# Kernel tuning notes

Measured on AMD Instinct MI355X. Metric: run time of the kernel, lower is better.

The kernel has to match this reference:

```python
import jax, jax.numpy as jnp
import numpy as np

N = 50000   # nodes
E = 800000  # edges
D = 128     # hidden_dim
O = 128     # out_dim (must equal hidden_dim; see prior_mean Linear)
T = 16      # number of timesteps for the modeled time encoding
EPS = 1e-9


def _gcn(x, W, b, src, dst, ew, n):
    """PyG-style GCNConv: add self-loops, symmetric deg^-1/2 normalization."""
    loop = jnp.arange(n)
    s = jnp.concatenate([src, loop])
    d = jnp.concatenate([dst, loop])
    w = jnp.concatenate([ew, jnp.ones((n,), x.dtype)])
    deg = jax.ops.segment_sum(w, d, num_segments=n)
    dinv = jnp.where(deg > 0, jax.lax.rsqrt(deg), 0.0)
    norm = dinv[s] * w * dinv[d]              # [E+N]
    h = x @ W                                  # [N, out]
    out = jax.ops.segment_sum(h[s] * norm[:, None], d, num_segments=n)
    return out + b


def setup_inputs() -> dict:
    key = jax.random.key(0)
    ks = jax.random.split(key, 20)

    def lin(k, fan_in, fan_out):
        return jax.random.normal(k, (fan_in, fan_out), jnp.float32) / np.sqrt(fan_in)

    return {
        "edge_index": jax.random.randint(ks[0], (2, E), 0, N, dtype=jnp.int64),
        "x": jax.random.normal(ks[1], (N, D), jnp.float32),
        "t": 3,
        "edge_score": jax.random.uniform(ks[2], (E,), jnp.float32),
        "total_len": 16,
        "train_len": 12,
        "W_enc": lin(ks[3], D, D), "b_enc": jnp.zeros((D,), jnp.float32),
        "W_mu": lin(ks[4], D, O), "b_mu": jnp.zeros((O,), jnp.float32),
        "W_std": lin(ks[5], D, O), "b_std": jnp.zeros((O,), jnp.float32),
        "W_prior": lin(ks[6], D, O), "b_prior": jnp.zeros((O,), jnp.float32),
        "W_pm": lin(ks[7], D, O), "b_pm": jnp.zeros((O,), jnp.float32),
        "W_ps": lin(ks[8], D, O), "b_ps": jnp.zeros((O,), jnp.float32),
        "time_emb": 0.02 * jax.random.normal(ks[9], (T, O), jnp.float32),
    }


def reference(edge_index, x, t, edge_score, total_len, train_len,
              W_enc, b_enc, W_mu, b_mu, W_std, b_std,
              W_prior, b_prior, W_pm, b_pm, W_ps, b_ps, time_emb):
    src, dst = edge_index[0], edge_index[1]
    n = x.shape[0]
    ones_e = jnp.ones((src.shape[0],), x.dtype)

    # encoder
    enc_t = jax.nn.relu(_gcn(x, W_enc, b_enc, src, dst, edge_score, n))
    # drop = 0.0 -> dropout is identity
    enc_mean_t = _gcn(enc_t, W_mu, b_mu, src, dst, ones_e, n)
    enc_std_t = jax.nn.sigmoid(_gcn(enc_t, W_std, b_std, src, dst, ones_e, n))

    # reparameterize (fixed eps for determinism)
    eps = jax.random.normal(jax.random.key(42), enc_mean_t.shape, enc_mean_t.dtype)
    conf_z_t = eps * enc_std_t + enc_mean_t

    # prior branch: time_encoding(prior, t) modeled as additive time embedding
    prior = jax.nn.relu(_gcn(x, W_prior, b_prior, src, dst, ones_e, n))
    prior = prior + time_emb[t]
    prior_mean = prior @ W_pm + b_pm
    prior_std = jax.nn.sigmoid(prior @ W_ps + b_ps)

    # fused KL divergence
    kl = (2.0 * jnp.log(prior_std + EPS) - 2.0 * jnp.log(enc_std_t + EPS)
          + ((enc_std_t + EPS) ** 2 + (enc_mean_t - prior_mean) ** 2)
          / (prior_std + EPS) ** 2 - 1.0)
    kl_loss = 0.5 * jnp.mean(jnp.sum(kl, axis=1), axis=0)
    return kl_loss, conf_z_t
```

## Files before the change

### kernel.cpp

```cpp
#include <hip/hip_runtime.h>
#include <math.h>

#define D 128

typedef unsigned int u32;
typedef unsigned short u16;
typedef __attribute__((ext_vector_type(8))) short bf16x8;
typedef __attribute__((ext_vector_type(4))) float f32x4;
typedef __attribute__((ext_vector_type(4))) u32 u32x4;

__device__ __forceinline__ u32 rotl32(u32 x, int r){ return (x<<r) | (x>>(32-r)); }

__device__ __forceinline__ u16 f2bf(float x){
  u32 u = __float_as_uint(x);
  return (u16)((u + 0x7fffu + ((u >> 16) & 1u)) >> 16);
}
__device__ __forceinline__ float bf2f(u16 h){ return __uint_as_float(((u32)h) << 16); }

__device__ __forceinline__ float jax_normal_part_xor(u32 m){
  const u32 ks0 = 0u, ks1 = 42u, ks2 = 0x1BD11BF0u;
  u32 x0 = 0u + ks0;
  u32 x1 = m  + ks1;
  #define TF_R4(a,b,c,d) \
    x0 += x1; x1 = rotl32(x1,(a)); x1 ^= x0; \
    x0 += x1; x1 = rotl32(x1,(b)); x1 ^= x0; \
    x0 += x1; x1 = rotl32(x1,(c)); x1 ^= x0; \
    x0 += x1; x1 = rotl32(x1,(d)); x1 ^= x0;
  TF_R4(13,15,26,6)   x0 += ks1; x1 += ks2 + 1u;
  TF_R4(17,29,16,24)  x0 += ks2; x1 += ks0 + 2u;
  TF_R4(13,15,26,6)   x0 += ks0; x1 += ks1 + 3u;
  TF_R4(17,29,16,24)  x0 += ks1; x1 += ks2 + 4u;
  TF_R4(13,15,26,6)   x0 += ks2; x1 += ks0 + 5u;
  #undef TF_R4
  u32 bits = x0 ^ x1;
  float f = __uint_as_float((bits >> 9) | 0x3F800000u) - 1.0f;
  const float LO = -0.99999994f;
  float u = fmaxf(LO, f * 2.0f + LO);
  float w = -__logf(fmaf(-u, u, 1.0f));
  float p;
  if (w < 5.0f){
    w -= 2.5f;
    p =  2.81022636e-08f;
    p = fmaf(p, w,  3.43273939e-07f);
    p = fmaf(p, w, -3.5233877e-06f);
    p = fmaf(p, w, -4.39150654e-06f);
    p = fmaf(p, w,  0.00021858087f);
    p = fmaf(p, w, -0.00125372503f);
    p = fmaf(p, w, -0.00417768164f);
    p = fmaf(p, w,  0.246640727f);
    p = fmaf(p, w,  1.50140941f);
  } else {
    w = sqrtf(w) - 3.0f;
    p = -0.000200214257f;
    p = fmaf(p, w,  0.000100950558f);
    p = fmaf(p, w,  0.00134934322f);
    p = fmaf(p, w, -0.00367342844f);
    p = fmaf(p, w,  0.00573950773f);
    p = fmaf(p, w, -0.0076224613f);
    p = fmaf(p, w,  0.00943887047f);
    p = fmaf(p, w,  1.00167406f);
    p = fmaf(p, w,  2.83297682f);
  }
  return 1.41421354f * (p * u);
}

__device__ __forceinline__ float sigmoidf_(float z){ return 1.0f / (1.0f + __expf(-z)); }

__global__ void k_detect(const u32* __restrict__ e_u32, int* __restrict__ flag){
  __shared__ int s_nz;
  if (threadIdx.x == 0) s_nz = 0;
  __syncthreads();
  if (e_u32[2*threadIdx.x + 1] != 0u) atomicAdd(&s_nz, 1);
  __syncthreads();
  if (threadIdx.x == 0) *flag = (s_nz == 0) ? 1 : 0;
}

__global__ void k_norm(const void* __restrict__ eidx, const int* __restrict__ flag,
                       int* __restrict__ src_w, int* __restrict__ dst_w, int e){
  int i = blockIdx.x*256 + threadIdx.x;
  if (i >= e) return;
  if (*flag){
    const u32* u = (const u32*)eidx;
    src_w[i] = (int)u[2*(size_t)i];
    dst_w[i] = (int)u[2*((size_t)e + i)];
  } else {
    const int* p = (const int*)eidx;
    src_w[i] = p[i];
    dst_w[i] = p[e + i];
  }
}

__global__ void k_init(int* __restrict__ cnt, int n){
  int i = blockIdx.x*256 + threadIdx.x;
  if (i < n) cnt[i] = 0;
}

__global__ void k_hist(const int* __restrict__ dst, int* __restrict__ cnt, int e){
  int i = blockIdx.x*256 + threadIdx.x;
  if (i >= e) return;
  atomicAdd(&cnt[dst[i]], 1);
}

__global__ __launch_bounds__(256) void k_scan1(const int* __restrict__ cnt,
                                               int* __restrict__ rp,
                                               int* __restrict__ bsum, int n){
  __shared__ int sh[256];
  int tid = threadIdx.x, idx = blockIdx.x*256 + tid;
  int v = (idx < n) ? cnt[idx] : 0;
  sh[tid] = v; __syncthreads();
  for (int off = 1; off < 256; off <<= 1){
    int t = (tid >= off) ? sh[tid-off] : 0;
    __syncthreads(); sh[tid] += t; __syncthreads();
  }
  if (idx < n) rp[idx] = sh[tid] - v;
  if (tid == 255) bsum[blockIdx.x] = sh[255];
}

__global__ __launch_bounds__(1024) void k_scan2(int* __restrict__ bsum, int nb){
  __shared__ int sh[1024];
  int tid = threadIdx.x;
  int v = (tid < nb) ? bsum[tid] : 0;
  sh[tid] = v; __syncthreads();
  for (int off = 1; off < 1024; off <<= 1){
    int t = (tid >= off) ? sh[tid-off] : 0;
    __syncthreads(); sh[tid] += t; __syncthreads();
  }
  if (tid < nb) bsum[tid] = sh[tid] - v;
}

__global__ void k_scan3(int* __restrict__ rp, int* __restrict__ cur,
                        const int* __restrict__ bsum, const int* __restrict__ cnt,
                        float* __restrict__ dinv_o, int n, int e){
  int idx = blockIdx.x*256 + threadIdx.x;
  if (idx < n){
    int r = rp[idx] + bsum[blockIdx.x];
    rp[idx] = r; cur[idx] = r;
    dinv_o[idx] = rsqrtf((float)(cnt[idx] + 1));
  }
  if (idx == 0) rp[n] = e;
}

__global__ void k_scatter(const int* __restrict__ src, const int* __restrict__ dst,
                          const float* __restrict__ sc, int* __restrict__ cur,
                          int* __restrict__ col, float* __restrict__ wsrt, int e){
  int i = blockIdx.x*256 + threadIdx.x;
  if (i >= e) return;
  int d = dst[i];
  int p = atomicAdd(&cur[d], 1);
  col[p] = src[i];
  wsrt[p] = sc[i];
}

__global__ void k_deg(const int* __restrict__ rp, const float* __restrict__ wsrt,
                      float* __restrict__ dinv_s, int n){
  int i = blockIdx.x*256 + threadIdx.x;
  if (i >= n) return;
  float s = 1.0f;
  int e0 = rp[i], e1 = rp[i+1];
  for (int j = e0; j < e1; ++j) s += wsrt[j];
  dinv_s[i] = rsqrtf(s);
}

__global__ void k_wconv(const float* __restrict__ W0, const float* __restrict__ W1,
                        const float* __restrict__ W2, const float* __restrict__ W3,
                        const float* __restrict__ W4, const float* __restrict__ W5,
                        u16* __restrict__ wt){
  const float* Ws[6] = {W0,W1,W2,W3,W4,W5};
  const float* W = Ws[blockIdx.y];
  u16* Wt = wt + (size_t)blockIdx.y*16384;
  int idx = blockIdx.x*256 + threadIdx.x;
  int k = idx >> 7, col = idx & 127;
  Wt[col*128 + k] = f2bf(W[idx]);
}

__global__ __launch_bounds__(256) void k_agg_dual(
    const float* __restrict__ x, const int* __restrict__ rp,
    const int* __restrict__ col, const float* __restrict__ wsrt,
    const float* __restrict__ dinv_s, const float* __restrict__ dinv_o,
    u16* __restrict__ out_s, u16* __restrict__ out_o, int n){
  int wid = (blockIdx.x * 256 + threadIdx.x) >> 6;
  int lane = threadIdx.x & 63;
  if (wid >= n) return;
  const float2* x2 = (const float2*)x;
  float dsv = dinv_s[wid], dov = dinv_o[wid];
  float2 xv = x2[(size_t)wid*64 + lane];
  float ss = dsv*dsv, oo = dov*dov;
  float2 as = { xv.x*ss, xv.y*ss };
  float2 ao = { xv.x*oo, xv.y*oo };
  int e0 = rp[wid], e1 = rp[wid+1];
  for (int base = e0; base < e1; base += 64){
    int cnt = e1 - base; if (cnt > 64) cnt = 64;
    int idx = base + (lane < cnt ? lane : cnt - 1);
    int   sl = col[idx];
    float wl = wsrt[idx];
    float nsl = dinv_s[sl] * wl * dsv;
    float nol = dinv_o[sl] * dov;
    int j = 0;
    for (; j + 4 <= cnt; j += 4){
      int   s0=__shfl(sl,j),   s1=__shfl(sl,j+1),   s2=__shfl(sl,j+2),   s3=__shfl(sl,j+3);
      float a0=__shfl(nsl,j),  a1=__shfl(nsl,j+1),  a2=__shfl(nsl,j+2),  a3=__shfl(nsl,j+3);
      float b0=__shfl(nol,j),  b1=__shfl(nol,j+1),  b2=__shfl(nol,j+2),  b3=__shfl(nol,j+3);
      float2 r0 = x2[(size_t)s0*64 + lane];
      float2 r1 = x2[(size_t)s1*64 + lane];
      float2 r2 = x2[(size_t)s2*64 + lane];
      float2 r3 = x2[(size_t)s3*64 + lane];
      as.x = fmaf(a0,r0.x,as.x); as.y = fmaf(a0,r0.y,as.y);
      ao.x = fmaf(b0,r0.x,ao.x); ao.y = fmaf(b0,r0.y,ao.y);
      as.x = fmaf(a1,r1.x,as.x); as.y = fmaf(a1,r1.y,as.y);
      ao.x = fmaf(b1,r1.x,ao.x); ao.y = fmaf(b1,r1.y,ao.y);
      as.x = fmaf(a2,r2.x,as.x); as.y = fmaf(a2,r2.y,as.y);
      ao.x = fmaf(b2,r2.x,ao.x); ao.y = fmaf(b2,r2.y,ao.y);
      as.x = fmaf(a3,r3.x,as.x); as.y = fmaf(a3,r3.y,as.y);
      ao.x = fmaf(b3,r3.x,ao.x); ao.y = fmaf(b3,r3.y,ao.y);
    }
    for (; j < cnt; ++j){
      int   s0=__shfl(sl,j);
      float a0=__shfl(nsl,j), b0=__shfl(nol,j);
      float2 r0 = x2[(size_t)s0*64 + lane];
      as.x = fmaf(a0,r0.x,as.x); as.y = fmaf(a0,r0.y,as.y);
      ao.x = fmaf(b0,r0.x,ao.x); ao.y = fmaf(b0,r0.y,ao.y);
    }
  }
  ((u32*)out_s)[(size_t)wid*64 + lane] = (u32)f2bf(as.x) | ((u32)f2bf(as.y) << 16);
  ((u32*)out_o)[(size_t)wid*64 + lane] = (u32)f2bf(ao.x) | ((u32)f2bf(ao.y) << 16);
}

__global__ __launch_bounds__(256) void k_agg_one(
    const u16* __restrict__ h, const int* __restrict__ rp,
    const int* __restrict__ col, const float* __restrict__ dinv_o,
    u16* __restrict__ out, int n){
  int wid = (blockIdx.x * 256 + threadIdx.x) >> 6;
  int lane = threadIdx.x & 63;
  if (wid >= n) return;
  const u32* h2 = (const u32*)h;
  float dov = dinv_o[wid];
  u32 hv = h2[(size_t)wid*64 + lane];
  float oo = dov*dov;
  float2 ao = { bf2f((u16)(hv & 0xffff))*oo, bf2f((u16)(hv >> 16))*oo };
  int e0 = rp[wid], e1 = rp[wid+1];
  for (int base = e0; base < e1; base += 64){
    int cnt = e1 - base; if (cnt > 64) cnt = 64;
    int idx = base + (lane < cnt ? lane : cnt - 1);
    int   sl = col[idx];
    float nol = dinv_o[sl] * dov;
    int j = 0;
    for (; j + 4 <= cnt; j += 4){
      int   s0=__shfl(sl,j),  s1=__shfl(sl,j+1),  s2=__shfl(sl,j+2),  s3=__shfl(sl,j+3);
      float b0=__shfl(nol,j), b1=__shfl(nol,j+1), b2=__shfl(nol,j+2), b3=__shfl(nol,j+3);
      u32 r0 = h2[(size_t)s0*64 + lane];
      u32 r1 = h2[(size_t)s1*64 + lane];
      u32 r2 = h2[(size_t)s2*64 + lane];
      u32 r3 = h2[(size_t)s3*64 + lane];
      ao.x = fmaf(b0, bf2f((u16)(r0&0xffff)), ao.x); ao.y = fmaf(b0, bf2f((u16)(r0>>16)), ao.y);
      ao.x = fmaf(b1, bf2f((u16)(r1&0xffff)), ao.x); ao.y = fmaf(b1, bf2f((u16)(r1>>16)), ao.y);
      ao.x = fmaf(b2, bf2f((u16)(r2&0xffff)), ao.x); ao.y = fmaf(b2, bf2f((u16)(r2>>16)), ao.y);
      ao.x = fmaf(b3, bf2f((u16)(r3&0xffff)), ao.x); ao.y = fmaf(b3, bf2f((u16)(r3>>16)), ao.y);
    }
    for (; j < cnt; ++j){
      int   s0=__shfl(sl,j);
      float b0=__shfl(nol,j);
      u32 r0 = h2[(size_t)s0*64 + lane];
      ao.x = fmaf(b0, bf2f((u16)(r0&0xffff)), ao.x); ao.y = fmaf(b0, bf2f((u16)(r0>>16)), ao.y);
    }
  }
  ((u32*)out)[(size_t)wid*64 + lane] = (u32)f2bf(ao.x) | ((u32)f2bf(ao.y) << 16);
}


__global__ __launch_bounds__(256) void k_mfma_act2(
    const u16* __restrict__ A0, const u16* __restrict__ Wt0, const float* __restrict__ b0,
    const u16* __restrict__ A1, const u16* __restrict__ Wt1, const float* __restrict__ b1,
    const float* __restrict__ temb, const int* __restrict__ t_ptr,
    u16* __restrict__ out0, u16* __restrict__ out1, int n){
  const int sl = blockIdx.y;
  const u16* A  = sl ? A1 : A0;
  const u16* Wt = sl ? Wt1 : Wt0;
  const float* b = sl ? b1 : b0;
  u16* out = sl ? out1 : out0;
  const int tid = threadIdx.x;
  const int lane = tid & 63, wave = tid >> 6;
  const int lr = lane & 15, lg = lane >> 4;
  const int row0 = blockIdx.x * 64;
  int rowf = row0 + wave*16 + lr;
  int rowc = rowf < n ? rowf : n - 1;
  const char* Arow = (const char*)A + (size_t)rowc*256;
  const char* Wb   = (const char*)Wt + lg*16;
  f32x4 z = {0.f,0.f,0.f,0.f};
  f32x4 acc[8];
  #pragma unroll
  for (int i = 0; i < 8; ++i) acc[i] = z;
  #pragma unroll
  for (int ks = 0; ks < 4; ++ks){
    bf16x8 a = *(const bf16x8*)(Arow + ks*64 + lg*16);
    #pragma unroll
    for (int cf = 0; cf < 8; ++cf){
      bf16x8 bb = *(const bf16x8*)(Wb + (cf*16 + lr)*256 + ks*64);
      acc[cf] = __builtin_amdgcn_mfma_f32_16x16x32_bf16(a, bb, acc[cf], 0, 0, 0);
    }
  }
  int t = sl ? *t_ptr : 0;
  int rbase = row0 + wave*16 + (lg << 2);
  #pragma unroll
  for (int cf = 0; cf < 8; ++cf){
    int colw = cf*16 + lr;
    float bb = b[colw];
    float tt = sl ? temb[t*128 + colw] : 0.f;
    #pragma unroll
    for (int r = 0; r < 4; ++r){
      int row = rbase + r;
      if (row < n)
        out[(size_t)row*128 + colw] = f2bf(fmaxf(acc[cf][r] + bb, 0.f) + tt);
    }
  }
}

__global__ __launch_bounds__(256) void k_mfma_dual(
    const u16* __restrict__ A, const u16* __restrict__ Wt1, const float* __restrict__ b1,
    const u16* __restrict__ Wt2, const float* __restrict__ b2,
    u32* __restrict__ pmps, int n){
  const int tid = threadIdx.x;
  const int lane = tid & 63, wave = tid >> 6;
  const int lr = lane & 15, lg = lane >> 4;
  const int row0 = blockIdx.x * 64;
  int rowf = row0 + wave*16 + lr;
  int rowc = rowf < n ? rowf : n - 1;
  const char* Arow = (const char*)A + (size_t)rowc*256;
  const char* W1b  = (const char*)Wt1 + lg*16;
  const char* W2b  = (const char*)Wt2 + lg*16;
  f32x4 z = {0.f,0.f,0.f,0.f};
  f32x4 acc1[8], acc2[8];
  #pragma unroll
  for (int i = 0; i < 8; ++i){ acc1[i] = z; acc2[i] = z; }
  #pragma unroll
  for (int ks = 0; ks < 4; ++ks){
    bf16x8 a = *(const bf16x8*)(Arow + ks*64 + lg*16);
    #pragma unroll
    for (int cf = 0; cf < 8; ++cf){
      int off = (cf*16 + lr)*256 + ks*64;
      bf16x8 bb1 = *(const bf16x8*)(W1b + off);
      acc1[cf] = __builtin_amdgcn_mfma_f32_16x16x32_bf16(a, bb1, acc1[cf], 0, 0, 0);
      bf16x8 bb2 = *(const bf16x8*)(W2b + off);
      acc2[cf] = __builtin_amdgcn_mfma_f32_16x16x32_bf16(a, bb2, acc2[cf], 0, 0, 0);
    }
  }
  int rbase = row0 + wave*16 + (lg << 2);
  #pragma unroll
  for (int cf = 0; cf < 8; ++cf){
    int colw = cf*16 + lr;
    float bb1 = b1[colw], bb2 = b2[colw];
    #pragma unroll
    for (int r = 0; r < 4; ++r){
      int row = rbase + r;
      if (row < n){
        u16 pmh = f2bf(acc1[cf][r] + bb1);
        u16 psh = f2bf(sigmoidf_(acc2[cf][r] + bb2));
        pmps[(size_t)row*128 + colw] = (u32)pmh | ((u32)psh << 16);
      }
    }
  }
}

__global__ __launch_bounds__(256) void k_mfma_final(
    const u16* __restrict__ A, const u16* __restrict__ Wtmu, const float* __restrict__ bmu,
    const u16* __restrict__ Wtstd, const float* __restrict__ bstd,
    const u32* __restrict__ pmps,
    float* __restrict__ conf, float* __restrict__ pblk, int n){
  const int tid = threadIdx.x;
  const int lane = tid & 63, wave = tid >> 6;
  const int lr = lane & 15, lg = lane >> 4;
  const int row0 = blockIdx.x * 64;
  int rowf = row0 + wave*16 + lr;
  int rowc = rowf < n ? rowf : n - 1;
  const char* Arow = (const char*)A + (size_t)rowc*256;
  const char* W1b  = (const char*)Wtmu + lg*16;
  const char* W2b  = (const char*)Wtstd + lg*16;
  f32x4 z = {0.f,0.f,0.f,0.f};
  f32x4 acc1[8], acc2[8];
  #pragma unroll
  for (int i = 0; i < 8; ++i){ acc1[i] = z; acc2[i] = z; }
  #pragma unroll
  for (int ks = 0; ks < 4; ++ks){
    bf16x8 a = *(const bf16x8*)(Arow + ks*64 + lg*16);
    #pragma unroll
    for (int cf = 0; cf < 8; ++cf){
      int off = (cf*16 + lr)*256 + ks*64;
      bf16x8 bb1 = *(const bf16x8*)(W1b + off);
      acc1[cf] = __builtin_amdgcn_mfma_f32_16x16x32_bf16(a, bb1, acc1[cf], 0, 0, 0);
      bf16x8 bb2 = *(const bf16x8*)(W2b + off);
      acc2[cf] = __builtin_amdgcn_mfma_f32_16x16x32_bf16(a, bb2, acc2[cf], 0, 0, 0);
    }
  }
  const float EPS = 1e-9f;
  int rbase = row0 + wave*16 + (lg << 2);
  float klsum = 0.f;
  #pragma unroll
  for (int cf = 0; cf < 8; ++cf){
    int colw = cf*16 + lr;
    float bb1 = bmu[colw], bb2 = bstd[colw];
    #pragma unroll
    for (int r = 0; r < 4; ++r){
      int row = rbase + r;
      if (row < n){
        size_t m = (size_t)row*128 + colw;
        float em = acc1[cf][r] + bb1;
        float es = sigmoidf_(acc2[cf][r] + bb2);
        float eps = jax_normal_part_xor((u32)m);
        conf[m] = fmaf(eps, es, em);
        u32 pp = pmps[m];
        float pmv = bf2f((u16)(pp & 0xffff)), psv = bf2f((u16)(pp >> 16));
        float es_e = es + EPS, ps_e = psv + EPS;
        float diff = em - pmv;
        klsum += 2.0f*__logf(ps_e/es_e)
               + (es_e*es_e + diff*diff) / (ps_e*ps_e) - 1.0f;
      }
    }
  }
  #pragma unroll
  for (int off = 32; off > 0; off >>= 1) klsum += __shfl_down(klsum, off);
  __shared__ float wsum[4];
  if ((tid & 63) == 0) wsum[tid >> 6] = klsum;
  __syncthreads();
  if (tid == 0) pblk[blockIdx.x] = wsum[0] + wsum[1] + wsum[2] + wsum[3];
}

__global__ __launch_bounds__(256) void k_finish(const float* __restrict__ pblk, int nb,
                                                float* __restrict__ out0, int n){
  __shared__ double sh[256];
  double s = 0.0;
  for (int i = threadIdx.x; i < nb; i += 256) s += (double)pblk[i];
  sh[threadIdx.x] = s; __syncthreads();
  for (int off = 128; off > 0; off >>= 1){
    if (threadIdx.x < off) sh[threadIdx.x] += sh[threadIdx.x + off];
    __syncthreads();
  }
  if (threadIdx.x == 0) out0[0] = (float)(0.5 * sh[0] / (double)n);
}

extern "C" void kernel_launch(void* const* d_in, const int* in_sizes, int n_in,
                              void* d_out, int out_size, void* d_ws, size_t ws_size,
                              hipStream_t stream){
  const void*  eidx   = d_in[0];
  const float* x      = (const float*)d_in[1];
  const int*   t_ptr  = (const int*)d_in[2];
  const float* escore = (const float*)d_in[3];
  const float* W_enc = (const float*)d_in[6];  const float* b_enc = (const float*)d_in[7];
  const float* W_mu  = (const float*)d_in[8];  const float* b_mu  = (const float*)d_in[9];
  const float* W_std = (const float*)d_in[10]; const float* b_std = (const float*)d_in[11];
  const float* W_pr  = (const float*)d_in[12]; const float* b_pr  = (const float*)d_in[13];
  const float* W_pm  = (const float*)d_in[14]; const float* b_pm  = (const float*)d_in[15];
  const float* W_ps  = (const float*)d_in[16]; const float* b_ps  = (const float*)d_in[17];
  const float* temb  = (const float*)d_in[18];

  const int N = in_sizes[1] / D;
  const int E = in_sizes[3];

  char* w = (char*)d_ws;
  auto alloc = [&](size_t bytes) -> char* {
    char* p = w; w += (bytes + 255) & ~(size_t)255; return p;
  };
  int*    flag   = (int*)   alloc(256);
  int*    src_w  = (int*)   alloc((size_t)E*4);
  int*    dst_w  = (int*)   alloc((size_t)E*4);
  int*    cnt    = (int*)   alloc((size_t)N*4);
  int*    rp     = (int*)   alloc((size_t)(N+1)*4);
  int*    cur    = (int*)   alloc((size_t)N*4);
  float*  dinv_s = (float*) alloc((size_t)N*4);
  float*  dinv_o = (float*) alloc((size_t)N*4);
  int*    bsum   = (int*)   alloc(1024*4);
  int*    col    = (int*)   alloc((size_t)E*4);
  float*  wsrt   = (float*) alloc((size_t)E*4);
  u16*    wt     = (u16*)   alloc((size_t)6*16384*2);
  u16*    B1     = (u16*)   alloc((size_t)N*D*2);
  u16*    B2     = (u16*)   alloc((size_t)N*D*2);
  u16*    B3     = (u16*)   alloc((size_t)N*D*2);
  u32*    PMPS   = (u32*)   alloc((size_t)N*D*4);
  u16*    B5     = (u16*)   alloc((size_t)N*D*2);
  const int gG64 = (N + 63) / 64;
  float*  pblk   = (float*) alloc((size_t)gG64*4);
  (void)ws_size; (void)n_in; (void)out_size;

  float* conf = ((float*)d_out) + 1;

  u16* Wt_enc = wt + 0*16384;
  u16* Wt_pr  = wt + 1*16384;
  u16* Wt_pm  = wt + 2*16384;
  u16* Wt_ps  = wt + 3*16384;
  u16* Wt_mu  = wt + 4*16384;
  u16* Wt_std = wt + 5*16384;

  const int gE  = (E + 255) / 256;
  const int gN  = (N + 255) / 256;
  const int gW  = (N * 64 + 255) / 256;

  k_wconv <<<dim3(64,6), 256, 0, stream>>>(W_enc, W_pr, W_pm, W_ps, W_mu, W_std, wt);
  k_detect <<<1, 256, 0, stream>>>((const u32*)eidx, flag);
  k_norm   <<<gE, 256, 0, stream>>>(eidx, flag, src_w, dst_w, E);
  k_init   <<<gN, 256, 0, stream>>>(cnt, N);
  k_hist   <<<gE, 256, 0, stream>>>(dst_w, cnt, E);
  k_scan1  <<<gN, 256, 0, stream>>>(cnt, rp, bsum, N);
  k_scan2  <<<1, 1024, 0, stream>>>(bsum, gN);
  k_scan3  <<<gN, 256, 0, stream>>>(rp, cur, bsum, cnt, dinv_o, N, E);
  k_scatter<<<gE, 256, 0, stream>>>(src_w, dst_w, escore, cur, col, wsrt, E);
  k_deg    <<<gN, 256, 0, stream>>>(rp, wsrt, dinv_s, N);

  k_agg_dual<<<gW, 256, 0, stream>>>(x, rp, col, wsrt, dinv_s, dinv_o, B1, B2, N);
  k_mfma_act2<<<dim3(gG64,2), 256, 0, stream>>>(B1, Wt_enc, b_enc, B2, Wt_pr, b_pr,
                                                temb, t_ptr, B3, B5, N);
  k_agg_one<<<gW, 256, 0, stream>>>(B3, rp, col, dinv_o, B2, N);
  k_mfma_dual<<<gG64, 256, 0, stream>>>(B5, Wt_pm, b_pm, Wt_ps, b_ps, PMPS, N);
  k_mfma_final<<<gG64, 256, 0, stream>>>(B2, Wt_mu, b_mu, Wt_std, b_std, PMPS,
                                         conf, pblk, N);
  k_finish<<<1, 256, 0, stream>>>(pblk, gG64, (float*)d_out, N);
}
```

Before: 384.3 us.

## Fuse prior head GEMMs into KL kernel and precompute bf16 noise

Merges the prior mean/std GEMM kernel into the final KL kernel so the packed prior buffer is no longer written and re-read. Moves the Threefry normal-noise generation into a separate kernel that stores eps as packed bf16, and retiles the MFMA kernels to 32 rows per block with waves split across column halves. This adds an extra eps buffer write and read and rounds the noise to bf16, reducing accuracy of conf_z.

```diff
diff --git a/kernel.cpp b/kernel.cpp
--- a/kernel.cpp
+++ b/kernel.cpp
@@ -66,6 +66,17 @@
 
 __device__ __forceinline__ float sigmoidf_(float z){ return 1.0f / (1.0f + __expf(-z)); }
 
+__global__ __launch_bounds__(256) void k_eps(u32* __restrict__ epsb, int half_total){
+  int idx = blockIdx.x*256 + threadIdx.x;
+  int stride = gridDim.x*256;
+  for (int i = idx; i < half_total; i += stride){
+    u32 m0 = 2u*(u32)i;
+    float e0 = jax_normal_part_xor(m0);
+    float e1 = jax_normal_part_xor(m0 + 1u);
+    epsb[i] = (u32)f2bf(e0) | ((u32)f2bf(e1) << 16);
+  }
+}
+
 __global__ void k_detect(const u32* __restrict__ e_u32, int* __restrict__ flag){
   __shared__ int s_nz;
   if (threadIdx.x == 0) s_nz = 0;
@@ -280,29 +291,30 @@
   const int tid = threadIdx.x;
   const int lane = tid & 63, wave = tid >> 6;
   const int lr = lane & 15, lg = lane >> 4;
-  const int row0 = blockIdx.x * 64;
-  int rowf = row0 + wave*16 + lr;
+  const int rw = wave >> 1, cw = wave & 1;
+  const int row0 = blockIdx.x*32 + rw*16;
+  int rowf = row0 + lr;
   int rowc = rowf < n ? rowf : n - 1;
   const char* Arow = (const char*)A + (size_t)rowc*256;
-  const char* Wb   = (const char*)Wt + lg*16;
+  const char* Wb   = (const char*)Wt + (cw*64 + lr)*256 + lg*16;
   f32x4 z = {0.f,0.f,0.f,0.f};
-  f32x4 acc[8];
-  #pragma unroll
-  for (int i = 0; i < 8; ++i) acc[i] = z;
+  f32x4 acc[4];
+  #pragma unroll
+  for (int i = 0; i < 4; ++i) acc[i] = z;
   #pragma unroll
   for (int ks = 0; ks < 4; ++ks){
     bf16x8 a = *(const bf16x8*)(Arow + ks*64 + lg*16);
     #pragma unroll
-    for (int cf = 0; cf < 8; ++cf){
-      bf16x8 bb = *(const bf16x8*)(Wb + (cf*16 + lr)*256 + ks*64);
+    for (int cf = 0; cf < 4; ++cf){
+      bf16x8 bb = *(const bf16x8*)(Wb + cf*16*256 + ks*64);
       acc[cf] = __builtin_amdgcn_mfma_f32_16x16x32_bf16(a, bb, acc[cf], 0, 0, 0);
     }
   }
   int t = sl ? *t_ptr : 0;
-  int rbase = row0 + wave*16 + (lg << 2);
-  #pragma unroll
-  for (int cf = 0; cf < 8; ++cf){
-    int colw = cf*16 + lr;
+  int rbase = row0 + (lg << 2);
+  #pragma unroll
+  for (int cf = 0; cf < 4; ++cf){
+    int colw = cw*64 + cf*16 + lr;
     float bb = b[colw];
     float tt = sl ? temb[t*128 + colw] : 0.f;
     #pragma unroll
@@ -314,100 +326,65 @@
   }
 }
 
-__global__ __launch_bounds__(256) void k_mfma_dual(
-    const u16* __restrict__ A, const u16* __restrict__ Wt1, const float* __restrict__ b1,
-    const u16* __restrict__ Wt2, const float* __restrict__ b2,
-    u32* __restrict__ pmps, int n){
-  const int tid = threadIdx.x;
-  const int lane = tid & 63, wave = tid >> 6;
-  const int lr = lane & 15, lg = lane >> 4;
-  const int row0 = blockIdx.x * 64;
-  int rowf = row0 + wave*16 + lr;
-  int rowc = rowf < n ? rowf : n - 1;
-  const char* Arow = (const char*)A + (size_t)rowc*256;
-  const char* W1b  = (const char*)Wt1 + lg*16;
-  const char* W2b  = (const char*)Wt2 + lg*16;
-  f32x4 z = {0.f,0.f,0.f,0.f};
-  f32x4 acc1[8], acc2[8];
-  #pragma unroll
-  for (int i = 0; i < 8; ++i){ acc1[i] = z; acc2[i] = z; }
-  #pragma unroll
-  for (int ks = 0; ks < 4; ++ks){
-    bf16x8 a = *(const bf16x8*)(Arow + ks*64 + lg*16);
-    #pragma unroll
-    for (int cf = 0; cf < 8; ++cf){
-      int off = (cf*16 + lr)*256 + ks*64;
-      bf16x8 bb1 = *(const bf16x8*)(W1b + off);
-      acc1[cf] = __builtin_amdgcn_mfma_f32_16x16x32_bf16(a, bb1, acc1[cf], 0, 0, 0);
-      bf16x8 bb2 = *(const bf16x8*)(W2b + off);
-      acc2[cf] = __builtin_amdgcn_mfma_f32_16x16x32_bf16(a, bb2, acc2[cf], 0, 0, 0);
-    }
-  }
-  int rbase = row0 + wave*16 + (lg << 2);
-  #pragma unroll
-  for (int cf = 0; cf < 8; ++cf){
-    int colw = cf*16 + lr;
-    float bb1 = b1[colw], bb2 = b2[colw];
-    #pragma unroll
-    for (int r = 0; r < 4; ++r){
-      int row = rbase + r;
-      if (row < n){
-        u16 pmh = f2bf(acc1[cf][r] + bb1);
-        u16 psh = f2bf(sigmoidf_(acc2[cf][r] + bb2));
-        pmps[(size_t)row*128 + colw] = (u32)pmh | ((u32)psh << 16);
-      }
-    }
-  }
-}
-
-__global__ __launch_bounds__(256) void k_mfma_final(
-    const u16* __restrict__ A, const u16* __restrict__ Wtmu, const float* __restrict__ bmu,
-    const u16* __restrict__ Wtstd, const float* __restrict__ bstd,
-    const u32* __restrict__ pmps,
+__global__ __launch_bounds__(256) void k_mfma_quad(
+    const u16* __restrict__ Apr, const u16* __restrict__ Aen,
+    const u16* __restrict__ Wtpm, const float* __restrict__ bpm,
+    const u16* __restrict__ Wtps, const float* __restrict__ bps,
+    const u16* __restrict__ Wtmu, const float* __restrict__ bmu,
+    const u16* __restrict__ Wtsd, const float* __restrict__ bsd,
+    const u32* __restrict__ epsb,
     float* __restrict__ conf, float* __restrict__ pblk, int n){
   const int tid = threadIdx.x;
   const int lane = tid & 63, wave = tid >> 6;
   const int lr = lane & 15, lg = lane >> 4;
-  const int row0 = blockIdx.x * 64;
-  int rowf = row0 + wave*16 + lr;
+  const int rw = wave >> 1, cw = wave & 1;
+  const int row0 = blockIdx.x*32 + rw*16;
+  int rowf = row0 + lr;
   int rowc = rowf < n ? rowf : n - 1;
-  const char* Arow = (const char*)A + (size_t)rowc*256;
-  const char* W1b  = (const char*)Wtmu + lg*16;
-  const char* W2b  = (const char*)Wtstd + lg*16;
+  const char* Ap = (const char*)Apr + (size_t)rowc*256;
+  const char* Ae = (const char*)Aen + (size_t)rowc*256;
+  const int wcb = (cw*64 + lr)*256 + lg*16;
+  const char* Wpm = (const char*)Wtpm + wcb;
+  const char* Wps = (const char*)Wtps + wcb;
+  const char* Wmu = (const char*)Wtmu + wcb;
+  const char* Wsd = (const char*)Wtsd + wcb;
   f32x4 z = {0.f,0.f,0.f,0.f};
-  f32x4 acc1[8], acc2[8];
-  #pragma unroll
-  for (int i = 0; i < 8; ++i){ acc1[i] = z; acc2[i] = z; }
+  f32x4 aPM[4], aPS[4], aMU[4], aSD[4];
+  #pragma unroll
+  for (int i = 0; i < 4; ++i){ aPM[i]=z; aPS[i]=z; aMU[i]=z; aSD[i]=z; }
   #pragma unroll
   for (int ks = 0; ks < 4; ++ks){
-    bf16x8 a = *(const bf16x8*)(Arow + ks*64 + lg*16);
+    bf16x8 a5 = *(const bf16x8*)(Ap + ks*64 + lg*16);
+    bf16x8 a2 = *(const bf16x8*)(Ae + ks*64 + lg*16);
     #pragma unroll
-    for (int cf = 0; cf < 8; ++cf){
-      int off = (cf*16 + lr)*256 + ks*64;
-      bf16x8 bb1 = *(const bf16x8*)(W1b + off);
-      acc1[cf] = __builtin_amdgcn_mfma_f32_16x16x32_bf16(a, bb1, acc1[cf], 0, 0, 0);
-      bf16x8 bb2 = *(const bf16x8*)(W2b + off);
-      acc2[cf] = __builtin_amdgcn_mfma_f32_16x16x32_bf16(a, bb2, acc2[cf], 0, 0, 0);
+    for (int cf = 0; cf < 4; ++cf){
+      int off = cf*16*256 + ks*64;
+      aPM[cf] = __builtin_amdgcn_mfma_f32_16x16x32_bf16(a5, *(const bf16x8*)(Wpm+off), aPM[cf], 0,0,0);
+      aPS[cf] = __builtin_amdgcn_mfma_f32_16x16x32_bf16(a5, *(const bf16x8*)(Wps+off), aPS[cf], 0,0,0);
+      aMU[cf] = __builtin_amdgcn_mfma_f32_16x16x32_bf16(a2, *(const bf16x8*)(Wmu+off), aMU[cf], 0,0,0);
+      aSD[cf] = __builtin_amdgcn_mfma_f32_16x16x32_bf16(a2, *(const bf16x8*)(Wsd+off), aSD[cf], 0,0,0);
     }
   }
   const float EPS = 1e-9f;
-  int rbase = row0 + wave*16 + (lg << 2);
+  int rbase = row0 + (lg << 2);
   float klsum = 0.f;
   #pragma unroll
-  for (int cf = 0; cf < 8; ++cf){
-    int colw = cf*16 + lr;
-    float bb1 = bmu[colw], bb2 = bstd[colw];
+  for (int cf = 0; cf < 4; ++cf){
+    int colw = cw*64 + cf*16 + lr;
+    float bb1 = bpm[colw], bb2 = bps[colw];
+    float bb3 = bmu[colw], bb4 = bsd[colw];
     #pragma unroll
     for (int r = 0; r < 4; ++r){
       int row = rbase + r;
       if (row < n){
         size_t m = (size_t)row*128 + colw;
-        float em = acc1[cf][r] + bb1;
-        float es = sigmoidf_(acc2[cf][r] + bb2);
-        float eps = jax_normal_part_xor((u32)m);
+        float pmv = aPM[cf][r] + bb1;
+        float psv = sigmoidf_(aPS[cf][r] + bb2);
+        float em  = aMU[cf][r] + bb3;
+        float es  = sigmoidf_(aSD[cf][r] + bb4);
+        u32 ew = epsb[m >> 1];
+        float eps = bf2f((u16)((colw & 1) ? (ew >> 16) : (ew & 0xffff)));
         conf[m] = fmaf(eps, es, em);
-        u32 pp = pmps[m];
-        float pmv = bf2f((u16)(pp & 0xffff)), psv = bf2f((u16)(pp >> 16));
         float es_e = es + EPS, ps_e = psv + EPS;
         float diff = em - pmv;
         klsum += 2.0f*__logf(ps_e/es_e)
@@ -473,10 +450,10 @@
   u16*    B1     = (u16*)   alloc((size_t)N*D*2);
   u16*    B2     = (u16*)   alloc((size_t)N*D*2);
   u16*    B3     = (u16*)   alloc((size_t)N*D*2);
-  u32*    PMPS   = (u32*)   alloc((size_t)N*D*4);
   u16*    B5     = (u16*)   alloc((size_t)N*D*2);
-  const int gG64 = (N + 63) / 64;
-  float*  pblk   = (float*) alloc((size_t)gG64*4);
+  u32*    EPSB   = (u32*)   alloc((size_t)N*64*4);
+  const int gG32 = (N + 31) / 32;
+  float*  pblk   = (float*) alloc((size_t)gG32*4);
   (void)ws_size; (void)n_in; (void)out_size;
 
   float* conf = ((float*)d_out) + 1;
@@ -492,7 +469,8 @@
   const int gN  = (N + 255) / 256;
   const int gW  = (N * 64 + 255) / 256;
 
-  k_wconv <<<dim3(64,6), 256, 0, stream>>>(W_enc, W_pr, W_pm, W_ps, W_mu, W_std, wt);
+  k_eps    <<<2048, 256, 0, stream>>>(EPSB, N*64);
+  k_wconv  <<<dim3(64,6), 256, 0, stream>>>(W_enc, W_pr, W_pm, W_ps, W_mu, W_std, wt);
   k_detect <<<1, 256, 0, stream>>>((const u32*)eidx, flag);
   k_norm   <<<gE, 256, 0, stream>>>(eidx, flag, src_w, dst_w, E);
   k_init   <<<gN, 256, 0, stream>>>(cnt, N);
@@ -504,11 +482,11 @@
   k_deg    <<<gN, 256, 0, stream>>>(rp, wsrt, dinv_s, N);
 
   k_agg_dual<<<gW, 256, 0, stream>>>(x, rp, col, wsrt, dinv_s, dinv_o, B1, B2, N);
-  k_mfma_act2<<<dim3(gG64,2), 256, 0, stream>>>(B1, Wt_enc, b_enc, B2, Wt_pr, b_pr,
+  k_mfma_act2<<<dim3(gG32,2), 256, 0, stream>>>(B1, Wt_enc, b_enc, B2, Wt_pr, b_pr,
                                                 temb, t_ptr, B3, B5, N);
   k_agg_one<<<gW, 256, 0, stream>>>(B3, rp, col, dinv_o, B2, N);
-  k_mfma_dual<<<gG64, 256, 0, stream>>>(B5, Wt_pm, b_pm, Wt_ps, b_ps, PMPS, N);
-  k_mfma_final<<<gG64, 256, 0, stream>>>(B2, Wt_mu, b_mu, Wt_std, b_std, PMPS,
-                                         conf, pblk, N);
-  k_finish<<<1, 256, 0, stream>>>(pblk, gG64, (float*)d_out, N);
-}
+  k_mfma_quad<<<gG32, 256, 0, stream>>>(B5, B2, Wt_pm, b_pm, Wt_ps, b_ps,
+                                        Wt_mu, b_mu, Wt_std, b_std, EPSB,
+                                        conf, pblk, N);
+  k_finish<<<1, 256, 0, stream>>>(pblk, gG32, (float*)d_out, N);
+}
```

After: 337.7 us. 12.1% less time.
